# Performance work log

Hardware: AMD Instinct MI355X
Metric: run time of the kernel (lower is better)

## Reference

```python
import jax, jax.numpy as jnp
import numpy as np

B, S, D, H = 4, 1024, 1024, 16
HD = D // H  # head dim = 64
SCALE = 1.0 / float(np.sqrt(HD))
W_INIT = 0.02


def setup_inputs() -> dict:
    key = jax.random.key(0)
    ks = jax.random.split(key, 8)
    f = lambda k, shape: jax.random.normal(k, shape, dtype=jnp.float32)
    return {
        "q": f(ks[0], (B, S, D)),
        "k": f(ks[1], (B, S, D)),
        "v": f(ks[2], (B, S, D)),
        "Wq": f(ks[3], (D, D)) * W_INIT, "bq": jnp.zeros((D,), jnp.float32),
        "Wk": f(ks[4], (D, D)) * W_INIT, "bk": jnp.zeros((D,), jnp.float32),
        "Wv": f(ks[5], (D, D)) * W_INIT, "bv": jnp.zeros((D,), jnp.float32),
        "Wo": f(ks[6], (D, D)) * W_INIT, "bo": jnp.zeros((D,), jnp.float32),
    }


def _split_heads(x):
    # [B, S, D] -> [B, H, S, HD]
    return x.reshape(B, S, H, HD).transpose(0, 2, 1, 3)


def reference(q, k, v, Wq, bq, Wk, bk, Wv, bv, Wo, bo):
    # linear input projections (torch Linear: x @ W.T + b)
    qh = _split_heads(q @ Wq.T + bq) * SCALE
    kh = _split_heads(k @ Wk.T + bk)
    vh = _split_heads(v @ Wv.T + bv)
    # scaled dot-product attention, full score matrix as in the source
    scores = jnp.einsum("bhqd,bhkd->bhqk", qh, kh)  # [B,H,S,S]
    weights = jax.nn.softmax(scores, axis=-1)
    ctx = jnp.einsum("bhqk,bhkd->bhqd", weights, vh)  # [B,H,S,HD]
    ctx = ctx.transpose(0, 2, 1, 3).reshape(B, S, D)
    # output projection (dropout=0, activation=None -> identity)
    return ctx @ Wo.T + bo
```

## Files before the change

### kernel.cpp

```cpp
#include <hip/hip_runtime.h>
#include <hip/hip_bf16.h>

typedef __attribute__((ext_vector_type(8))) short short8;
typedef __attribute__((ext_vector_type(4))) float f32x4;

static __device__ __forceinline__ short f2bf(float x) {
    __hip_bfloat16 h(x);
    return __builtin_bit_cast(short, h);
}

static __device__ __forceinline__ void gload16(const void* g, void* l) {
    auto* gp = reinterpret_cast<const __attribute__((address_space(1))) unsigned*>(
        reinterpret_cast<uintptr_t>(g));
    auto* lp = reinterpret_cast<__attribute__((address_space(3))) unsigned*>(
        reinterpret_cast<uintptr_t>(l));
    __builtin_amdgcn_global_load_lds(gp, lp, 16, 0, 0);
}

static __device__ __forceinline__ unsigned cvt_pk_bf16(float lo, float hi) {
    unsigned r;
    asm("v_cvt_pk_bf16_f32 %0, %1, %2" : "=v"(r) : "v"(lo), "v"(hi));
    return r;
}

__global__ __launch_bounds__(256) void convert_all(
    const float* __restrict__ q, const float* __restrict__ k, const float* __restrict__ v,
    const float* __restrict__ Wq, const float* __restrict__ Wk,
    const float* __restrict__ Wv, const float* __restrict__ Wo,
    short* __restrict__ abf_q, short* __restrict__ abf_k, short* __restrict__ abf_v,
    short* __restrict__ wbf)
{
    const int blk = blockIdx.x;
    const float* src;
    short* dst;
    size_t off;
    if (blk < 6144) {
        const int seg = blk >> 11;
        src = (seg == 0) ? q : (seg == 1) ? k : v;
        dst = (seg == 0) ? abf_q : (seg == 1) ? abf_k : abf_v;
        off = ((size_t)(blk & 2047) * 256 + threadIdx.x) * 8;
    } else {
        const int wseg = (blk - 6144) >> 9;
        src = (wseg == 0) ? Wq : (wseg == 1) ? Wk : (wseg == 2) ? Wv : Wo;
        dst = wbf + (size_t)wseg * 1048576;
        off = ((size_t)((blk - 6144) & 511) * 256 + threadIdx.x) * 8;
    }
    float4 f0 = *(const float4*)(src + off);
    float4 f1 = *(const float4*)(src + off + 4);
    short8 o;
    o[0] = f2bf(f0.x); o[1] = f2bf(f0.y); o[2] = f2bf(f0.z); o[3] = f2bf(f0.w);
    o[4] = f2bf(f1.x); o[5] = f2bf(f1.y); o[6] = f2bf(f1.z); o[7] = f2bf(f1.w);
    *(short8*)(dst + off) = o;
}

__global__ __launch_bounds__(256) void proj_qkv_kernel(
    const short* __restrict__ abf_q, const short* __restrict__ abf_k,
    const short* __restrict__ abf_v, const short* __restrict__ wbf,
    const float* __restrict__ bq, const float* __restrict__ bk, const float* __restrict__ bv,
    short* __restrict__ qh, short* __restrict__ kh, short* __restrict__ vt)
{
    const int z = blockIdx.z;
    const short* A    = (z == 0) ? abf_q : (z == 1) ? abf_k : abf_v;
    const short* W    = wbf + (size_t)z * 1048576;
    const float* bias = (z == 0) ? bq : (z == 1) ? bk : bv;

    __shared__ __align__(16) short As[128 * 64];
    __shared__ __align__(16) short Bs[128 * 64];

    const int tid = threadIdx.x;
    const int lane = tid & 63;
    const int w = tid >> 6;
    const int wr = w >> 1, wc = w & 1;
    const int row0 = blockIdx.x * 128;
    const int col0 = blockIdx.y * 128;
    const int fr = lane & 15;
    const int g = lane >> 4;
    const int frs = fr & 7;
    const int srow = lane >> 3;
    const int sch  = ((lane & 7) ^ srow) * 8;

    f32x4 acc[4][4] = {};

    for (int t = 0; t < 16; ++t) {
        const int k0 = t * 64;
        #pragma unroll
        for (int i = 0; i < 4; ++i) {
            const int r0 = w * 32 + i * 8;
            gload16(A + (size_t)(row0 + r0 + srow) * 1024 + k0 + sch, &As[r0 * 64]);
            gload16(W + (size_t)(col0 + r0 + srow) * 1024 + k0 + sch, &Bs[r0 * 64]);
        }
        __syncthreads();
        #pragma unroll
        for (int kk = 0; kk < 2; ++kk) {
            short8 aF[4], bF[4];
            #pragma unroll
            for (int m = 0; m < 4; ++m)
                aF[m] = *(const short8*)&As[(wr * 64 + m * 16 + fr) * 64 + (((kk * 4 + g) ^ frs) * 8)];
            #pragma unroll
            for (int n = 0; n < 4; ++n)
                bF[n] = *(const short8*)&Bs[(wc * 64 + n * 16 + fr) * 64 + (((kk * 4 + g) ^ frs) * 8)];
            if (z == 2) {
                #pragma unroll
                for (int m = 0; m < 4; ++m)
                    #pragma unroll
                    for (int n = 0; n < 4; ++n)
                        acc[m][n] = __builtin_amdgcn_mfma_f32_16x16x32_bf16(bF[n], aF[m], acc[m][n], 0, 0, 0);
            } else {
                #pragma unroll
                for (int m = 0; m < 4; ++m)
                    #pragma unroll
                    for (int n = 0; n < 4; ++n)
                        acc[m][n] = __builtin_amdgcn_mfma_f32_16x16x32_bf16(aF[m], bF[n], acc[m][n], 0, 0, 0);
            }
        }
        __syncthreads();
    }

    if (z == 2) {
        #pragma unroll
        for (int n = 0; n < 4; ++n) {
            #pragma unroll
            for (int i = 0; i < 4; ++i) {
                const int c = col0 + wc * 64 + n * 16 + g * 4 + i;
                const int h = c >> 6, hd = c & 63;
                const float bb = bias[c];
                #pragma unroll
                for (int m = 0; m < 4; ++m) {
                    const int r = row0 + wr * 64 + m * 16 + fr;
                    const int b = r >> 10, s = r & 1023;
                    vt[(((size_t)(b * 16 + h) * 64 + hd) << 10) + s] = f2bf(acc[m][n][i] + bb);
                }
            }
        }
    } else {
        short* out = (z == 0) ? qh : kh;
        const float scale = (z == 0) ? 0.1803368801111244f : 1.0f;
        #pragma unroll
        for (int n = 0; n < 4; ++n) {
            const int c = col0 + wc * 64 + n * 16 + fr;
            const int h = c >> 6, hd = c & 63;
            const float bb = bias[c];
            #pragma unroll
            for (int m = 0; m < 4; ++m) {
                #pragma unroll
                for (int i = 0; i < 4; ++i) {
                    const int r = row0 + wr * 64 + m * 16 + g * 4 + i;
                    const int b = r >> 10, s = r & 1023;
                    out[(((size_t)(b * 16 + h) * 1024 + s) << 6) + hd] =
                        f2bf((acc[m][n][i] + bb) * scale);
                }
            }
        }
    }
}

__global__ __launch_bounds__(256) void proj_o_kernel(
    const short* __restrict__ ctx, const short* __restrict__ wo,
    const float* __restrict__ bo, float* __restrict__ out)
{
    __shared__ __align__(16) short As[128 * 64];
    __shared__ __align__(16) short Bs[64 * 64];

    const int tid = threadIdx.x;
    const int lane = tid & 63;
    const int w = tid >> 6;
    const int row0 = blockIdx.x * 128;
    const int col0 = blockIdx.y * 64;
    const int fr = lane & 15;
    const int g = lane >> 4;
    const int frs = fr & 7;
    const int srow = lane >> 3;
    const int sch  = ((lane & 7) ^ srow) * 8;

    f32x4 acc[2][4] = {};

    for (int t = 0; t < 16; ++t) {
        const int k0 = t * 64;
        #pragma unroll
        for (int i = 0; i < 4; ++i) {
            const int r0 = w * 32 + i * 8;
            gload16(ctx + (size_t)(row0 + r0 + srow) * 1024 + k0 + sch, &As[r0 * 64]);
        }
        #pragma unroll
        for (int i = 0; i < 2; ++i) {
            const int r0 = w * 16 + i * 8;
            gload16(wo + (size_t)(col0 + r0 + srow) * 1024 + k0 + sch, &Bs[r0 * 64]);
        }
        __syncthreads();
        #pragma unroll
        for (int kk = 0; kk < 2; ++kk) {
            short8 aF[2], bF[4];
            #pragma unroll
            for (int m = 0; m < 2; ++m)
                aF[m] = *(const short8*)&As[(w * 32 + m * 16 + fr) * 64 + (((kk * 4 + g) ^ frs) * 8)];
            #pragma unroll
            for (int n = 0; n < 4; ++n)
                bF[n] = *(const short8*)&Bs[(n * 16 + fr) * 64 + (((kk * 4 + g) ^ frs) * 8)];
            #pragma unroll
            for (int m = 0; m < 2; ++m)
                #pragma unroll
                for (int n = 0; n < 4; ++n)
                    acc[m][n] = __builtin_amdgcn_mfma_f32_16x16x32_bf16(aF[m], bF[n], acc[m][n], 0, 0, 0);
        }
        __syncthreads();
    }

    #pragma unroll
    for (int n = 0; n < 4; ++n) {
        const int c = col0 + n * 16 + fr;
        const float bb = bo[c];
        #pragma unroll
        for (int m = 0; m < 2; ++m) {
            #pragma unroll
            for (int i = 0; i < 4; ++i) {
                const int r = row0 + w * 32 + m * 16 + g * 4 + i;
                out[(size_t)r * 1024 + c] = acc[m][n][i] + bb;
            }
        }
    }
}

__global__ __launch_bounds__(256) void attn_kernel(
    const short* __restrict__ qh, const short* __restrict__ kh,
    const short* __restrict__ vt, short* __restrict__ ctx)
{
    const int d = blockIdx.x;
    const int xcd = d & 7;
    const int s2 = d >> 3;
    const int bh = xcd * 8 + (s2 >> 4);
    const int qb = s2 & 15;
    const int b = bh >> 4, h = bh & 15;
    const int q0 = qb * 64;
    const short* Qh  = qh + (size_t)bh * 65536;
    const short* Kh  = kh + (size_t)bh * 65536;
    const short* Vth = vt + (size_t)bh * 65536;

    __shared__ __align__(16) short Ks[64 * 64];
    __shared__ __align__(16) short Vs[64 * 64];
    __shared__ __align__(16) short Pb[4][16 * 68];

    const int tid = threadIdx.x;
    const int lane = tid & 63;
    const int w = tid >> 6;
    const int fr = lane & 15;
    const int g = lane >> 4;
    const int fk = g * 8;
    const int frs = fr & 7;
    const int srow = lane >> 3;
    const int sch  = ((lane & 7) ^ srow) * 8;

    short8 qF[2];
    #pragma unroll
    for (int j = 0; j < 2; ++j)
        qF[j] = *(const short8*)(Qh + (q0 + w * 16 + fr) * 64 + j * 32 + fk);

    short8 onesF;
    #pragma unroll
    for (int j = 0; j < 8; ++j) onesF[j] = (short)0x3F80;

    f32x4 o[4] = {};
    f32x4 lacc = {};

    for (int kt = 0; kt < 16; ++kt) {
        const int kv0 = kt * 64;
        __syncthreads();
        #pragma unroll
        for (int i = 0; i < 2; ++i) {
            const int r0 = w * 16 + i * 8;
            gload16(Kh + (size_t)(kv0 + r0 + srow) * 64 + sch, &Ks[r0 * 64]);
            gload16(Vth + (size_t)(r0 + srow) * 1024 + kv0 + sch, &Vs[r0 * 64]);
        }
        __syncthreads();

        f32x4 sc[4] = {};
        __builtin_amdgcn_s_setprio(1);
        #pragma unroll
        for (int n = 0; n < 4; ++n) {
            const int r = n * 16 + fr;
            #pragma unroll
            for (int j = 0; j < 2; ++j) {
                short8 kF = *(const short8*)&Ks[r * 64 + (((j * 4 + g) ^ frs) * 8)];
                sc[n] = __builtin_amdgcn_mfma_f32_16x16x32_bf16(qF[j], kF, sc[n], 0, 0, 0);
            }
        }
        __builtin_amdgcn_s_setprio(0);

        {
            short* pbase = &Pb[w][(g * 4) * 68 + fr];
            #pragma unroll
            for (int n = 0; n < 4; ++n) {
                const unsigned u01 = cvt_pk_bf16(exp2f(sc[n][0]), exp2f(sc[n][1]));
                const unsigned u23 = cvt_pk_bf16(exp2f(sc[n][2]), exp2f(sc[n][3]));
                pbase[n * 16]       = (short)u01;
                pbase[n * 16 + 68]  = (short)(u01 >> 16);
                pbase[n * 16 + 136] = (short)u23;
                pbase[n * 16 + 204] = (short)(u23 >> 16);
            }
        }

        __builtin_amdgcn_s_setprio(1);
        #pragma unroll
        for (int half = 0; half < 2; ++half) {
            short8 pF = *(const short8*)&Pb[w][fr * 68 + half * 32 + fk];
            lacc = __builtin_amdgcn_mfma_f32_16x16x32_bf16(pF, onesF, lacc, 0, 0, 0);
            #pragma unroll
            for (int n = 0; n < 4; ++n) {
                short8 vF = *(const short8*)&Vs[(n * 16 + fr) * 64 + (((half * 4 + g) ^ frs) * 8)];
                o[n] = __builtin_amdgcn_mfma_f32_16x16x32_bf16(pF, vF, o[n], 0, 0, 0);
            }
        }
        __builtin_amdgcn_s_setprio(0);
    }

    float inv[4];
    #pragma unroll
    for (int i = 0; i < 4; ++i) inv[i] = 1.0f / lacc[i];
    #pragma unroll
    for (int n = 0; n < 4; ++n)
        #pragma unroll
        for (int i = 0; i < 4; ++i) {
            const int s = q0 + w * 16 + g * 4 + i;
            ctx[(size_t)(b * 1024 + s) * 1024 + h * 64 + n * 16 + fr] = f2bf(o[n][i] * inv[i]);
        }
}

extern "C" void kernel_launch(void* const* d_in, const int* in_sizes, int n_in,
                              void* d_out, int out_size, void* d_ws, size_t ws_size,
                              hipStream_t stream) {
    const float* q  = (const float*)d_in[0];
    const float* k  = (const float*)d_in[1];
    const float* v  = (const float*)d_in[2];
    const float* Wq = (const float*)d_in[3];
    const float* bq = (const float*)d_in[4];
    const float* Wk = (const float*)d_in[5];
    const float* bk = (const float*)d_in[6];
    const float* Wv = (const float*)d_in[7];
    const float* bv = (const float*)d_in[8];
    const float* Wo = (const float*)d_in[9];
    const float* bo = (const float*)d_in[10];

    char* ws = (char*)d_ws;
    const size_t SZ = (size_t)4096 * 1024 * 2;
    short* qh    = (short*)(ws);
    short* kh    = (short*)(ws + SZ);
    short* vt    = (short*)(ws + 2 * SZ);
    short* ctx   = (short*)(ws + 3 * SZ);
    short* abf_v = (short*)(ws + 4 * SZ);
    short* wbf   = (short*)(ws + 5 * SZ);
    short* abf_q = (short*)d_out;
    short* abf_k = (short*)d_out + 4194304;

    convert_all<<<8192, 256, 0, stream>>>(q, k, v, Wq, Wk, Wv, Wo,
                                          abf_q, abf_k, abf_v, wbf);
    proj_qkv_kernel<<<dim3(32, 8, 3), 256, 0, stream>>>(
        abf_q, abf_k, abf_v, wbf, bq, bk, bv, qh, kh, vt);
    attn_kernel<<<1024, 256, 0, stream>>>(qh, kh, vt, ctx);
    proj_o_kernel<<<dim3(32, 16), 256, 0, stream>>>(ctx, wbf + 3 * 1048576, bo, (float*)d_out);
}
```

Baseline: 206.4 us.

## Double-buffer LDS tiles in projection and attention kernels to overlap loads

Each of the three kernels gets a second shared-memory buffer for its K-loop tiles. The loads for the next tile are issued before the MFMA work on the current tile, and one barrier per iteration replaces the previous load-then-sync pattern. The aim is to hide global-to-LDS latency behind matrix compute. LDS use per block doubles, which may lower occupancy, most of all in the QKV projection kernel, now at 64KB.

```diff
diff --git a/kernel.cpp b/kernel.cpp
--- a/kernel.cpp
+++ b/kernel.cpp
@@ -64,8 +64,8 @@
     const short* W    = wbf + (size_t)z * 1048576;
     const float* bias = (z == 0) ? bq : (z == 1) ? bk : bv;
 
-    __shared__ __align__(16) short As[128 * 64];
-    __shared__ __align__(16) short Bs[128 * 64];
+    __shared__ __align__(16) short As[2][128 * 64];
+    __shared__ __align__(16) short Bs[2][128 * 64];
 
     const int tid = threadIdx.x;
     const int lane = tid & 63;
@@ -81,24 +81,34 @@
 
     f32x4 acc[4][4] = {};
 
+    #pragma unroll
+    for (int i = 0; i < 4; ++i) {
+        const int r0 = w * 32 + i * 8;
+        gload16(A + (size_t)(row0 + r0 + srow) * 1024 + sch, &As[0][r0 * 64]);
+        gload16(W + (size_t)(col0 + r0 + srow) * 1024 + sch, &Bs[0][r0 * 64]);
+    }
+    __syncthreads();
+
     for (int t = 0; t < 16; ++t) {
-        const int k0 = t * 64;
-        #pragma unroll
-        for (int i = 0; i < 4; ++i) {
-            const int r0 = w * 32 + i * 8;
-            gload16(A + (size_t)(row0 + r0 + srow) * 1024 + k0 + sch, &As[r0 * 64]);
-            gload16(W + (size_t)(col0 + r0 + srow) * 1024 + k0 + sch, &Bs[r0 * 64]);
-        }
-        __syncthreads();
+        const int cur = t & 1, nxt = cur ^ 1;
+        if (t < 15) {
+            const int k1 = (t + 1) * 64;
+            #pragma unroll
+            for (int i = 0; i < 4; ++i) {
+                const int r0 = w * 32 + i * 8;
+                gload16(A + (size_t)(row0 + r0 + srow) * 1024 + k1 + sch, &As[nxt][r0 * 64]);
+                gload16(W + (size_t)(col0 + r0 + srow) * 1024 + k1 + sch, &Bs[nxt][r0 * 64]);
+            }
+        }
         #pragma unroll
         for (int kk = 0; kk < 2; ++kk) {
             short8 aF[4], bF[4];
             #pragma unroll
             for (int m = 0; m < 4; ++m)
-                aF[m] = *(const short8*)&As[(wr * 64 + m * 16 + fr) * 64 + (((kk * 4 + g) ^ frs) * 8)];
+                aF[m] = *(const short8*)&As[cur][(wr * 64 + m * 16 + fr) * 64 + (((kk * 4 + g) ^ frs) * 8)];
             #pragma unroll
             for (int n = 0; n < 4; ++n)
-                bF[n] = *(const short8*)&Bs[(wc * 64 + n * 16 + fr) * 64 + (((kk * 4 + g) ^ frs) * 8)];
+                bF[n] = *(const short8*)&Bs[cur][(wc * 64 + n * 16 + fr) * 64 + (((kk * 4 + g) ^ frs) * 8)];
             if (z == 2) {
                 #pragma unroll
                 for (int m = 0; m < 4; ++m)
@@ -158,8 +168,8 @@
     const short* __restrict__ ctx, const short* __restrict__ wo,
     const float* __restrict__ bo, float* __restrict__ out)
 {
-    __shared__ __align__(16) short As[128 * 64];
-    __shared__ __align__(16) short Bs[64 * 64];
+    __shared__ __align__(16) short As[2][128 * 64];
+    __shared__ __align__(16) short Bs[2][64 * 64];
 
     const int tid = threadIdx.x;
     const int lane = tid & 63;
@@ -174,28 +184,42 @@
 
     f32x4 acc[2][4] = {};
 
+    #pragma unroll
+    for (int i = 0; i < 4; ++i) {
+        const int r0 = w * 32 + i * 8;
+        gload16(ctx + (size_t)(row0 + r0 + srow) * 1024 + sch, &As[0][r0 * 64]);
+    }
+    #pragma unroll
+    for (int i = 0; i < 2; ++i) {
+        const int r0 = w * 16 + i * 8;
+        gload16(wo + (size_t)(col0 + r0 + srow) * 1024 + sch, &Bs[0][r0 * 64]);
+    }
+    __syncthreads();
+
     for (int t = 0; t < 16; ++t) {
-        const int k0 = t * 64;
-        #pragma unroll
-        for (int i = 0; i < 4; ++i) {
-            const int r0 = w * 32 + i * 8;
-            gload16(ctx + (size_t)(row0 + r0 + srow) * 1024 + k0 + sch, &As[r0 * 64]);
-        }
-        #pragma unroll
-        for (int i = 0; i < 2; ++i) {
-            const int r0 = w * 16 + i * 8;
-            gload16(wo + (size_t)(col0 + r0 + srow) * 1024 + k0 + sch, &Bs[r0 * 64]);
-        }
-        __syncthreads();
+        const int cur = t & 1, nxt = cur ^ 1;
+        if (t < 15) {
+            const int k1 = (t + 1) * 64;
+            #pragma unroll
+            for (int i = 0; i < 4; ++i) {
+                const int r0 = w * 32 + i * 8;
+                gload16(ctx + (size_t)(row0 + r0 + srow) * 1024 + k1 + sch, &As[nxt][r0 * 64]);
+            }
+            #pragma unroll
+            for (int i = 0; i < 2; ++i) {
+                const int r0 = w * 16 + i * 8;
+                gload16(wo + (size_t)(col0 + r0 + srow) * 1024 + k1 + sch, &Bs[nxt][r0 * 64]);
+            }
+        }
         #pragma unroll
         for (int kk = 0; kk < 2; ++kk) {
             short8 aF[2], bF[4];
             #pragma unroll
             for (int m = 0; m < 2; ++m)
-                aF[m] = *(const short8*)&As[(w * 32 + m * 16 + fr) * 64 + (((kk * 4 + g) ^ frs) * 8)];
+                aF[m] = *(const short8*)&As[cur][(w * 32 + m * 16 + fr) * 64 + (((kk * 4 + g) ^ frs) * 8)];
             #pragma unroll
             for (int n = 0; n < 4; ++n)
-                bF[n] = *(const short8*)&Bs[(n * 16 + fr) * 64 + (((kk * 4 + g) ^ frs) * 8)];
+                bF[n] = *(const short8*)&Bs[cur][(n * 16 + fr) * 64 + (((kk * 4 + g) ^ frs) * 8)];
             #pragma unroll
             for (int m = 0; m < 2; ++m)
                 #pragma unroll
@@ -235,8 +259,8 @@
     const short* Kh  = kh + (size_t)bh * 65536;
     const short* Vth = vt + (size_t)bh * 65536;
 
-    __shared__ __align__(16) short Ks[64 * 64];
-    __shared__ __align__(16) short Vs[64 * 64];
+    __shared__ __align__(16) short Ks[2][64 * 64];
+    __shared__ __align__(16) short Vs[2][64 * 64];
     __shared__ __align__(16) short Pb[4][16 * 68];
 
     const int tid = threadIdx.x;
@@ -261,16 +285,25 @@
     f32x4 o[4] = {};
     f32x4 lacc = {};
 
+    #pragma unroll
+    for (int i = 0; i < 2; ++i) {
+        const int r0 = w * 16 + i * 8;
+        gload16(Kh + (size_t)(r0 + srow) * 64 + sch, &Ks[0][r0 * 64]);
+        gload16(Vth + (size_t)(r0 + srow) * 1024 + sch, &Vs[0][r0 * 64]);
+    }
+    __syncthreads();
+
     for (int kt = 0; kt < 16; ++kt) {
-        const int kv0 = kt * 64;
-        __syncthreads();
-        #pragma unroll
-        for (int i = 0; i < 2; ++i) {
-            const int r0 = w * 16 + i * 8;
-            gload16(Kh + (size_t)(kv0 + r0 + srow) * 64 + sch, &Ks[r0 * 64]);
-            gload16(Vth + (size_t)(r0 + srow) * 1024 + kv0 + sch, &Vs[r0 * 64]);
-        }
-        __syncthreads();
+        const int cur = kt & 1, nxt = cur ^ 1;
+        if (kt < 15) {
+            const int kv1 = (kt + 1) * 64;
+            #pragma unroll
+            for (int i = 0; i < 2; ++i) {
+                const int r0 = w * 16 + i * 8;
+                gload16(Kh + (size_t)(kv1 + r0 + srow) * 64 + sch, &Ks[nxt][r0 * 64]);
+                gload16(Vth + (size_t)(r0 + srow) * 1024 + kv1 + sch, &Vs[nxt][r0 * 64]);
+            }
+        }
 
         f32x4 sc[4] = {};
         __builtin_amdgcn_s_setprio(1);
@@ -279,7 +312,7 @@
             const int r = n * 16 + fr;
             #pragma unroll
             for (int j = 0; j < 2; ++j) {
-                short8 kF = *(const short8*)&Ks[r * 64 + (((j * 4 + g) ^ frs) * 8)];
+                short8 kF = *(const short8*)&Ks[cur][r * 64 + (((j * 4 + g) ^ frs) * 8)];
                 sc[n] = __builtin_amdgcn_mfma_f32_16x16x32_bf16(qF[j], kF, sc[n], 0, 0, 0);
             }
         }
@@ -305,11 +338,12 @@
             lacc = __builtin_amdgcn_mfma_f32_16x16x32_bf16(pF, onesF, lacc, 0, 0, 0);
             #pragma unroll
             for (int n = 0; n < 4; ++n) {
-                short8 vF = *(const short8*)&Vs[(n * 16 + fr) * 64 + (((half * 4 + g) ^ frs) * 8)];
+                short8 vF = *(const short8*)&Vs[cur][(n * 16 + fr) * 64 + (((half * 4 + g) ^ frs) * 8)];
                 o[n] = __builtin_amdgcn_mfma_f32_16x16x32_bf16(pF, vF, o[n], 0, 0, 0);
             }
         }
         __builtin_amdgcn_s_setprio(0);
+        __syncthreads();
     }
 
     float inv[4];
```

New measurement: 202.4 us. Within noise of the previous version (-1.9%).
